# Kernel optimization log

Measured on AMD Instinct MI355X. Metric: run time of the kernel, lower is better.

Reference implementation:

```python
import jax, jax.numpy as jnp
import numpy as np

# Module constants (match init_kwargs)
G = 8        # number of channel groups (len(list_input_dim))
D = 16       # per-group input dim
L = 1024     # sequence length
B = 16       # batch
E = 8        # num_experts
OUT = 64     # out_channels
KS = 3       # emb_kernel_size
K = 4        # hardcoded self.k in Channel_Embedding
LOSS_COEF = 0.01


def setup_inputs() -> dict:
    key = jax.random.key(0)
    k0, k1, k2, k3 = jax.random.split(key, 4)
    x = jax.random.normal(k0, (B, G * D, L), jnp.float32)
    # torch inits w_gate to zeros (degenerate); use small random weights for meaningful routing
    w_gate = jax.random.normal(k1, (G, D * 5, E), jnp.float32) * 0.1
    conv1_w = jax.random.normal(k2, (G, OUT, D, KS), jnp.float32) * (1.0 / np.sqrt(D * KS))
    conv1_b = jnp.zeros((G, OUT), jnp.float32)
    conv2_w = jax.random.normal(k3, (G, OUT * E, OUT, 1), jnp.float32) * (1.0 / np.sqrt(OUT))
    conv2_b = jnp.zeros((G, OUT * E), jnp.float32)
    return dict(x=x, w_gate=w_gate, conv1_w=conv1_w, conv1_b=conv1_b,
                conv2_w=conv2_w, conv2_b=conv2_b)


def _cv_squared(v):
    # torch: x.float().var() (unbiased) / (mean^2 + eps)
    v = v.astype(jnp.float32)
    return jnp.var(v, ddof=1) / (jnp.mean(v) ** 2 + 1e-10)


def _conv1d(x, w, b):
    # x [B,C,L], w [O,I,K] -> [B,O,L'] (VALID, stride 1)
    y = jax.lax.conv_general_dilated(x, w, (1,), 'VALID',
                                     dimension_numbers=('NCH', 'OIH', 'NCH'))
    return y + b[None, :, None]


def _group_forward(xg, wg, c1w, c1b, c2w, c2b):
    # xg: [B, D, L] single channel group
    Bb = xg.shape[0]
    # gating input: last timesteps [-6:-1] -> [B, D*5]
    gate_in = xg[:, :, -6:-1].reshape(Bb, -1)
    logits = jax.nn.softmax(gate_in @ wg, axis=1)           # [B, E]
    top_v, top_i = jax.lax.top_k(logits, min(K + 1, E))     # [B, K+1]
    tkv, tki = top_v[:, :K], top_i[:, :K]
    gk = tkv / (tkv.sum(1, keepdims=True) + 1e-6)
    gates = jnp.zeros_like(logits).at[jnp.arange(Bb)[:, None], tki].set(gk)  # [B, E]
    load = (gates > 0).sum(0)                               # eval path: _gates_to_load
    loss = _cv_squared(gates.sum(0)) + _cv_squared(load)
    # experts: conv(D->OUT, k=KS) -> tanh -> conv(OUT -> OUT*E, k=1)
    h = jnp.tanh(_conv1d(xg, c1w, c1b))
    raw = _conv1d(h, c2w, c2b)                              # [B, OUT*E, L']
    Lp = raw.shape[-1]
    # channel index = d*E + e (matches torch permute+reshape(B,-1,OUT,E))
    moe = jnp.einsum('bdel,be->bdl', raw.reshape(Bb, OUT, E, Lp), gates)  # [B, OUT, L']
    return moe, loss, gates


def reference(x, w_gate, conv1_w, conv1_b, conv2_w, conv2_b):
    # split channels into G groups of D: [G, B, D, L]
    xg = x.reshape(x.shape[0], G, D, x.shape[-1]).transpose(1, 0, 2, 3)
    moe, loss, gates = jax.vmap(_group_forward)(xg, w_gate, conv1_w, conv1_b, conv2_w, conv2_b)
    combine_features = moe.transpose(1, 0, 2, 3)   # [B, G, OUT, L']
    out_loss = LOSS_COEF * loss.sum()
    gates_out = gates.transpose(1, 2, 0)           # [B, E, G]
    return combine_features, out_loss, gates_out
```

## Files before the change

### kernel.cpp

```cpp
#include <hip/hip_runtime.h>
#include <hip/hip_bf16.h>

#define NG   8
#define ND   16
#define NL   1024
#define NB   16
#define NE   8
#define NOUT 64
#define NKS  3
#define NK   4
#define NLP  1022

#define OUT_LOSS  (NB*NG*NOUT*NLP)
#define OUT_GATES (OUT_LOSS + 1)

__device__ __forceinline__ float tanh_fast(float x) {
    float e = exp2f(x * 2.885390081777927f);
    return 1.0f - 2.0f / (e + 1.0f);
}

__device__ __forceinline__ void compute_gates_f(
    const float* __restrict__ x, const float* __restrict__ wg,
    int g, int b, float gates[8])
{
    float gi[80];
    const float* xrow = x + (size_t)(b * 128 + g * 16) * 1024 + (1024 - 6);
    #pragma unroll
    for (int d = 0; d < 16; ++d) {
        #pragma unroll
        for (int tt = 0; tt < 5; ++tt) gi[d * 5 + tt] = xrow[d * 1024 + tt];
    }

    float lg[8];
    #pragma unroll
    for (int e = 0; e < 8; ++e) lg[e] = 0.f;
    const float* wgg = wg + g * 640;
    #pragma unroll
    for (int j = 0; j < 80; ++j) {
        const float v = gi[j];
        #pragma unroll
        for (int e = 0; e < 8; ++e) lg[e] = fmaf(v, wgg[j * 8 + e], lg[e]);
    }

    float mx = lg[0];
    #pragma unroll
    for (int e = 1; e < 8; ++e) mx = fmaxf(mx, lg[e]);
    float s = 0.f;
    #pragma unroll
    for (int e = 0; e < 8; ++e) { lg[e] = expf(lg[e] - mx); s += lg[e]; }
    const float invsm = 1.f / s;
    #pragma unroll
    for (int e = 0; e < 8; ++e) lg[e] *= invsm;

    int used = 0;
    float tv[4]; int ti[4];
    #pragma unroll
    for (int k = 0; k < 4; ++k) {
        float bv = -1.f; int be = 0;
        #pragma unroll
        for (int e = 0; e < 8; ++e) {
            if (!((used >> e) & 1) && lg[e] > bv) { bv = lg[e]; be = e; }
        }
        tv[k] = bv; ti[k] = be; used |= (1 << be);
    }
    const float s4 = tv[0] + tv[1] + tv[2] + tv[3];
    const float invs = 1.f / (s4 + 1e-6f);
    #pragma unroll
    for (int e = 0; e < 8; ++e) {
        float v = 0.f;
        #pragma unroll
        for (int k = 0; k < 4; ++k) if (ti[k] == e) v = tv[k] * invs;
        gates[e] = v;
    }
}

__global__ __launch_bounds__(256) void prep_kernel(
    const float* __restrict__ x,   const float* __restrict__ wg,
    const float* __restrict__ c1w, const float* __restrict__ c2w,
    const float* __restrict__ c2b,
    float* __restrict__ out, float* __restrict__ weff,
    float* __restrict__ beff, float* __restrict__ w1r)
{
    const int bid = blockIdx.x;
    const int t   = threadIdx.x;

    __shared__ float glds[128][8];
    __shared__ float impa[64], loda[64];
    __shared__ float lossg[8];

    if (bid < 128) {
        const int gb = bid, g = gb >> 4, b = gb & 15;
        float gt[8];
        compute_gates_f(x, wg, g, b, gt);

        const int o  = t >> 2;
        const int iq = (t & 3) * 16;
        const float* w2g = c2w + (size_t)g * 512 * 64 + (size_t)o * 8 * 64 + iq;
        float acc[16];
        #pragma unroll
        for (int q = 0; q < 16; ++q) acc[q] = 0.f;
        #pragma unroll
        for (int e = 0; e < 8; ++e) {
            const float4* src = (const float4*)(w2g + e * 64);
            #pragma unroll
            for (int q = 0; q < 4; ++q) {
                float4 v = src[q];
                acc[q*4+0] = fmaf(gt[e], v.x, acc[q*4+0]);
                acc[q*4+1] = fmaf(gt[e], v.y, acc[q*4+1]);
                acc[q*4+2] = fmaf(gt[e], v.z, acc[q*4+2]);
                acc[q*4+3] = fmaf(gt[e], v.w, acc[q*4+3]);
            }
        }
        float4* dst = (float4*)(weff + (size_t)gb * 4096 + o * 64 + iq);
        #pragma unroll
        for (int q = 0; q < 4; ++q) {
            float4 v; v.x = acc[q*4+0]; v.y = acc[q*4+1];
                      v.z = acc[q*4+2]; v.w = acc[q*4+3];
            dst[q] = v;
        }
        if (t < 64) {
            const float* b2g = c2b + g * 512;
            float a = 0.f;
            #pragma unroll
            for (int e = 0; e < 8; ++e) a = fmaf(gt[e], b2g[t * 8 + e], a);
            beff[gb * 64 + t] = a;
        }
    } else if (bid < 136) {
        const int g = bid - 128;
        for (int idx = t; idx < 48 * 64; idx += 256) {
            const int j = idx >> 6, o = idx & 63;
            w1r[(size_t)(g * 48 + j) * 64 + o] = c1w[(size_t)g * 3072 + o * 48 + j];
        }
    } else {
        float gates[8];
        const int g = t >> 4, b = t & 15;
        if (t < 128) {
            compute_gates_f(x, wg, g, b, gates);
            #pragma unroll
            for (int e = 0; e < 8; ++e) {
                glds[t][e] = gates[e];
                out[OUT_GATES + (b * 8 + e) * 8 + g] = gates[e];
            }
        }
        __syncthreads();
        if (t < 64) {
            const int gg = t >> 3, e = t & 7;
            float si = 0.f, sl = 0.f;
            for (int bb = 0; bb < 16; ++bb) {
                const float v = glds[gg * 16 + bb][e];
                si += v;
                sl += (v > 0.f) ? 1.f : 0.f;
            }
            impa[t] = si; loda[t] = sl;
        }
        __syncthreads();
        if (t < 8) {
            float m1 = 0.f, m2 = 0.f;
            #pragma unroll
            for (int e = 0; e < 8; ++e) { m1 += impa[t * 8 + e]; m2 += loda[t * 8 + e]; }
            m1 *= 0.125f; m2 *= 0.125f;
            float v1 = 0.f, v2 = 0.f;
            #pragma unroll
            for (int e = 0; e < 8; ++e) {
                const float d1 = impa[t * 8 + e] - m1, d2 = loda[t * 8 + e] - m2;
                v1 += d1 * d1; v2 += d2 * d2;
            }
            v1 *= (1.f / 7.f); v2 *= (1.f / 7.f);
            lossg[t] = v1 / (m1 * m1 + 1e-10f) + v2 / (m2 * m2 + 1e-10f);
        }
        __syncthreads();
        if (t == 0) {
            float tot = 0.f;
            #pragma unroll
            for (int gg = 0; gg < 8; ++gg) tot += lossg[gg];
            out[OUT_LOSS] = 0.01f * tot;
        }
    }
}

__global__ __launch_bounds__(256, 4) void main_kernel(
    const float* __restrict__ x,    const float* __restrict__ w1r,
    const float* __restrict__ b1,   const float* __restrict__ weff,
    const float* __restrict__ beff, float* __restrict__ out)
{
    __shared__ float hT[64][128];

    const int bid   = blockIdx.x;
    const int tile  = bid & 7;
    const int gb    = bid >> 3;
    const int g     = gb >> 4, b = gb & 15;
    const int t     = threadIdx.x;
    const int lane  = t & 63;
    const int obase = __builtin_amdgcn_readfirstlane((t >> 6) << 4);
    const int c0    = lane * 2;
    const int l0    = tile * 128 + c0;
    const int lc    = (l0 <= NLP - 2) ? l0 : (NLP - 2);

    float a0[16], a1[16];
    const float* b1g = b1 + g * 64 + obase;
    #pragma unroll
    for (int o = 0; o < 16; ++o) { a0[o] = b1g[o]; a1[o] = a0[o]; }

    const float* xb  = x + (size_t)(b * 128 + g * 16) * 1024 + lc;
    const float* wrg = w1r + (size_t)(g * 48) * 64 + obase;
    #pragma unroll
    for (int i = 0; i < 16; ++i) {
        const float2 xa = *(const float2*)(xb + i * 1024);
        const float2 xc = *(const float2*)(xb + i * 1024 + 2);
        const float* wr = wrg + i * 192;
        #pragma unroll
        for (int o = 0; o < 16; ++o) {
            const float w0 = wr[o], w1 = wr[64 + o], w2 = wr[128 + o];
            a0[o] = fmaf(w0, xa.x, a0[o]);
            a0[o] = fmaf(w1, xa.y, a0[o]);
            a0[o] = fmaf(w2, xc.x, a0[o]);
            a1[o] = fmaf(w0, xa.y, a1[o]);
            a1[o] = fmaf(w1, xc.x, a1[o]);
            a1[o] = fmaf(w2, xc.y, a1[o]);
        }
    }
    #pragma unroll
    for (int o = 0; o < 16; ++o) {
        float2 hv; hv.x = tanh_fast(a0[o]); hv.y = tanh_fast(a1[o]);
        *(float2*)&hT[obase + o][c0] = hv;
    }

    __syncthreads();

    const float* bef = beff + gb * 64 + obase;
    #pragma unroll
    for (int o = 0; o < 16; ++o) { a0[o] = bef[o]; a1[o] = a0[o]; }

    const float* wef = weff + (size_t)gb * 4096 + (size_t)obase * 64;
    #pragma unroll
    for (int c = 0; c < 4; ++c) {
        float2 hh[16];
        #pragma unroll
        for (int i = 0; i < 16; ++i) hh[i] = *(const float2*)&hT[c * 16 + i][c0];
        #pragma unroll
        for (int o = 0; o < 16; ++o) {
            const float* wr = wef + o * 64 + c * 16;
            #pragma unroll
            for (int i = 0; i < 16; ++i) {
                a0[o] = fmaf(wr[i], hh[i].x, a0[o]);
                a1[o] = fmaf(wr[i], hh[i].y, a1[o]);
            }
        }
    }

    if (l0 <= NLP - 2) {
        float* ob = out + ((size_t)((b * 8 + g) * 64 + obase)) * NLP + l0;
        #pragma unroll
        for (int o = 0; o < 16; ++o) {
            float2 v; v.x = a0[o]; v.y = a1[o];
            *(float2*)(ob + (size_t)o * NLP) = v;
        }
    }
}

extern "C" void kernel_launch(void* const* d_in, const int* in_sizes, int n_in,
                              void* d_out, int out_size, void* d_ws, size_t ws_size,
                              hipStream_t stream) {
    const float* x   = (const float*)d_in[0];
    const float* wg  = (const float*)d_in[1];
    const float* c1w = (const float*)d_in[2];
    const float* c1b = (const float*)d_in[3];
    const float* c2w = (const float*)d_in[4];
    const float* c2b = (const float*)d_in[5];
    float* out = (float*)d_out;

    float* ws   = (float*)d_ws;
    float* beff = ws;
    float* weff = ws + 8192;
    float* w1r  = ws + 8192 + 524288;

    prep_kernel<<<137, 256, 0, stream>>>(x, wg, c1w, c2w, c2b, out, weff, beff, w1r);
    main_kernel<<<1024, 256, 0, stream>>>(x, w1r, c1b, weff, beff, out);
}
```

Before: 132.1 us.

## Remap blocks across XCDs and software-pipeline global and LDS loads

Block indices are remapped so that the eight sequence tiles of one (group,batch) pair land on the same XCD, which is meant to improve L2 reuse of the per-pair effective weights. The conv1 stage now issues all x loads up front in two batches before the FMA loops. The conv2 stage double-buffers the LDS reads of h, loading the next 16-channel chunk while the current one is consumed. The cost is higher register pressure under launch_bounds(256,4), which could cause spills or lower occupancy.

After: 125.7 us. 1.05x faster.

```diff
diff --git a/kernel.cpp b/kernel.cpp
--- a/kernel.cpp
+++ b/kernel.cpp
@@ -186,8 +186,10 @@
     __shared__ float hT[64][128];
 
     const int bid   = blockIdx.x;
-    const int tile  = bid & 7;
-    const int gb    = bid >> 3;
+    const int xcd   = bid & 7;
+    const int j     = bid >> 3;
+    const int gb    = ((j & 15) << 3) | xcd;
+    const int tile  = j >> 4;
     const int g     = gb >> 4, b = gb & 15;
     const int t     = threadIdx.x;
     const int lane  = t & 63;
@@ -203,20 +205,46 @@
 
     const float* xb  = x + (size_t)(b * 128 + g * 16) * 1024 + lc;
     const float* wrg = w1r + (size_t)(g * 48) * 64 + obase;
-    #pragma unroll
-    for (int i = 0; i < 16; ++i) {
-        const float2 xa = *(const float2*)(xb + i * 1024);
-        const float2 xc = *(const float2*)(xb + i * 1024 + 2);
+
+    float2 xaA[8], xcA[8];
+    #pragma unroll
+    for (int i = 0; i < 8; ++i) {
+        xaA[i] = *(const float2*)(xb + i * 1024);
+        xcA[i] = *(const float2*)(xb + i * 1024 + 2);
+    }
+    float2 xaB[8], xcB[8];
+    #pragma unroll
+    for (int i = 0; i < 8; ++i) {
+        xaB[i] = *(const float2*)(xb + (8 + i) * 1024);
+        xcB[i] = *(const float2*)(xb + (8 + i) * 1024 + 2);
+    }
+
+    #pragma unroll
+    for (int i = 0; i < 8; ++i) {
         const float* wr = wrg + i * 192;
         #pragma unroll
         for (int o = 0; o < 16; ++o) {
             const float w0 = wr[o], w1 = wr[64 + o], w2 = wr[128 + o];
-            a0[o] = fmaf(w0, xa.x, a0[o]);
-            a0[o] = fmaf(w1, xa.y, a0[o]);
-            a0[o] = fmaf(w2, xc.x, a0[o]);
-            a1[o] = fmaf(w0, xa.y, a1[o]);
-            a1[o] = fmaf(w1, xc.x, a1[o]);
-            a1[o] = fmaf(w2, xc.y, a1[o]);
+            a0[o] = fmaf(w0, xaA[i].x, a0[o]);
+            a0[o] = fmaf(w1, xaA[i].y, a0[o]);
+            a0[o] = fmaf(w2, xcA[i].x, a0[o]);
+            a1[o] = fmaf(w0, xaA[i].y, a1[o]);
+            a1[o] = fmaf(w1, xcA[i].x, a1[o]);
+            a1[o] = fmaf(w2, xcA[i].y, a1[o]);
+        }
+    }
+    #pragma unroll
+    for (int i = 0; i < 8; ++i) {
+        const float* wr = wrg + (8 + i) * 192;
+        #pragma unroll
+        for (int o = 0; o < 16; ++o) {
+            const float w0 = wr[o], w1 = wr[64 + o], w2 = wr[128 + o];
+            a0[o] = fmaf(w0, xaB[i].x, a0[o]);
+            a0[o] = fmaf(w1, xaB[i].y, a0[o]);
+            a0[o] = fmaf(w2, xcB[i].x, a0[o]);
+            a1[o] = fmaf(w0, xaB[i].y, a1[o]);
+            a1[o] = fmaf(w1, xcB[i].x, a1[o]);
+            a1[o] = fmaf(w2, xcB[i].y, a1[o]);
         }
     }
     #pragma unroll
@@ -232,19 +260,53 @@
     for (int o = 0; o < 16; ++o) { a0[o] = bef[o]; a1[o] = a0[o]; }
 
     const float* wef = weff + (size_t)gb * 4096 + (size_t)obase * 64;
-    #pragma unroll
-    for (int c = 0; c < 4; ++c) {
-        float2 hh[16];
-        #pragma unroll
-        for (int i = 0; i < 16; ++i) hh[i] = *(const float2*)&hT[c * 16 + i][c0];
-        #pragma unroll
-        for (int o = 0; o < 16; ++o) {
-            const float* wr = wef + o * 64 + c * 16;
-            #pragma unroll
-            for (int i = 0; i < 16; ++i) {
-                a0[o] = fmaf(wr[i], hh[i].x, a0[o]);
-                a1[o] = fmaf(wr[i], hh[i].y, a1[o]);
-            }
+
+    float2 hhA[16], hhB[16];
+    #pragma unroll
+    for (int i = 0; i < 16; ++i) hhA[i] = *(const float2*)&hT[i][c0];
+    #pragma unroll
+    for (int i = 0; i < 16; ++i) hhB[i] = *(const float2*)&hT[16 + i][c0];
+
+    #pragma unroll
+    for (int o = 0; o < 16; ++o) {
+        const float* wr = wef + o * 64;
+        #pragma unroll
+        for (int i = 0; i < 16; ++i) {
+            a0[o] = fmaf(wr[i], hhA[i].x, a0[o]);
+            a1[o] = fmaf(wr[i], hhA[i].y, a1[o]);
+        }
+    }
+    #pragma unroll
+    for (int i = 0; i < 16; ++i) hhA[i] = *(const float2*)&hT[32 + i][c0];
+
+    #pragma unroll
+    for (int o = 0; o < 16; ++o) {
+        const float* wr = wef + o * 64 + 16;
+        #pragma unroll
+        for (int i = 0; i < 16; ++i) {
+            a0[o] = fmaf(wr[i], hhB[i].x, a0[o]);
+            a1[o] = fmaf(wr[i], hhB[i].y, a1[o]);
+        }
+    }
+    #pragma unroll
+    for (int i = 0; i < 16; ++i) hhB[i] = *(const float2*)&hT[48 + i][c0];
+
+    #pragma unroll
+    for (int o = 0; o < 16; ++o) {
+        const float* wr = wef + o * 64 + 32;
+        #pragma unroll
+        for (int i = 0; i < 16; ++i) {
+            a0[o] = fmaf(wr[i], hhA[i].x, a0[o]);
+            a1[o] = fmaf(wr[i], hhA[i].y, a1[o]);
+        }
+    }
+    #pragma unroll
+    for (int o = 0; o < 16; ++o) {
+        const float* wr = wef + o * 64 + 48;
+        #pragma unroll
+        for (int i = 0; i < 16; ++i) {
+            a0[o] = fmaf(wr[i], hhB[i].x, a0[o]);
+            a1[o] = fmaf(wr[i], hhB[i].y, a1[o]);
         }
     }
 
```
